# Kernel optimization log

Measured on AMD Instinct MI355X. Metric: run time of the kernel, lower is better.

The kernel has to match this reference:

```python
import jax, jax.numpy as jnp
import numpy as np

G, M, H, HEADS, FFN, MAX_DIST, E = 8, 1024, 256, 8, 1024, 5, 131072
N = G * M
HD = H // HEADS

def _ln(x, g, b, eps=1e-5):
    m = x.mean(-1, keepdims=True)
    v = ((x - m) ** 2).mean(-1, keepdims=True)
    return (x - m) / jnp.sqrt(v + eps) * g + b

def _forward(x, gcn_w, gcn_b, qkv_w, qkv_b, proj_w, proj_b,
             ln1_g, ln1_b, ln2_g, ln2_b, ffn1_w, ffn1_b, ffn2_w, ffn2_b,
             bias_emb, oln1_g, oln1_b, oln2_g, oln2_b,
             offn1_w, offn1_b, offn2_w, offn2_b, edge_index, batch):
    src, dst = edge_index[0], edge_index[1]
    # --- local conv: GCNConv (self-loops + symmetric normalization) ---
    sl = jnp.arange(N, dtype=src.dtype)
    s2 = jnp.concatenate([src, sl]); d2 = jnp.concatenate([dst, sl])
    xw = x @ gcn_w.T
    deg = jax.ops.segment_sum(jnp.ones_like(d2, dtype=x.dtype), d2, num_segments=N)
    dinv = jnp.where(deg > 0, 1.0 / jnp.sqrt(deg), 0.0)
    norm = dinv[s2] * dinv[d2]
    x_local = jax.ops.segment_sum(xw[s2] * norm[:, None], d2, num_segments=N) + gcn_b
    # --- to_dense_batch ---
    counts = jax.ops.segment_sum(jnp.ones(N, jnp.int32), batch, num_segments=G)
    starts = jnp.concatenate([jnp.zeros(1, jnp.int32), jnp.cumsum(counts)[:-1]])
    local = jnp.arange(N, dtype=jnp.int32) - starts[batch]
    dense_x = jnp.zeros((G, M, H), x.dtype).at[batch, local].set(x)
    mask = jnp.zeros((G, M), bool).at[batch, local].set(True)
    # --- SPD via batched boolean adjacency powering (== per-node BFS capped at MAX_DIST) ---
    g_e = batch[src]
    valid = (batch[src] == batch[dst]) & (src != dst)
    ls, ld = local[src], local[dst]
    adj = jnp.zeros((G, M, M), bool).at[g_e, ls, ld].max(valid).at[g_e, ld, ls].max(valid)
    dist = jnp.full((G, M, M), MAX_DIST + 1, jnp.int32)
    eye = jnp.eye(M, dtype=bool)[None]
    dist = jnp.where(eye & mask[:, :, None], 0, dist)
    reach = adj
    dist = jnp.where(reach, jnp.minimum(dist, 1), dist)
    for d in range(2, MAX_DIST + 1):
        reach = jnp.einsum('gij,gjk->gik', reach.astype(x.dtype), adj.astype(x.dtype)) > 0
        dist = jnp.where(reach, jnp.minimum(dist, d), dist)
    attn_bias = bias_emb[dist][..., 0]  # [G, M, M]
    # --- Graphormer encoder layer (layers=1) ---
    h = dense_x
    qkv = (h @ qkv_w.T + qkv_b).reshape(G, M, 3, HEADS, HD).transpose(2, 0, 3, 1, 4)
    q, k, v = qkv[0], qkv[1], qkv[2]  # [G, heads, M, hd]
    scores = jnp.einsum('ghqd,ghkd->ghqk', q, k) * (HD ** -0.5)
    scores = scores + attn_bias[:, None].astype(scores.dtype)
    pad = ~mask
    scores = jnp.where(pad[:, None, None, :], -jnp.inf, scores)
    attn = jax.nn.softmax(scores, axis=-1)
    out = jnp.einsum('ghqk,ghkd->ghqd', attn, v).transpose(0, 2, 1, 3).reshape(G, M, H)
    out = out @ proj_w.T + proj_b
    h = _ln(h + out, ln1_g, ln1_b)
    ff = jax.nn.gelu(h @ ffn1_w.T + ffn1_b, approximate=False) @ ffn2_w.T + ffn2_b
    h = _ln(h + ff, ln2_g, ln2_b)
    h = jnp.where(pad[..., None], 0.0, h)
    x_global = h[batch, local]
    # --- GPS combine + outer FFN (dropout = identity at eval) ---
    y = _ln(x + (x_local + x_global), oln1_g, oln1_b)
    ff2 = jax.nn.gelu(y @ offn1_w.T + offn1_b, approximate=False) @ offn2_w.T + offn2_b
    return _ln(y + ff2, oln2_g, oln2_b)

def setup_inputs() -> dict:
    key = jax.random.key(0)
    ks = jax.random.split(key, 16)
    w = lambda k, *s: jax.random.normal(k, s, jnp.float32) * 0.02
    src = jax.random.randint(ks[0], (E,), 0, N, jnp.int32)
    # keep each edge inside one graph (graphs are contiguous blocks of M nodes)
    dst = (src // M) * M + jax.random.randint(ks[1], (E,), 0, M, jnp.int32)
    return dict(
        x=jax.random.normal(ks[2], (N, H), jnp.float32),
        gcn_w=w(ks[3], H, H), gcn_b=jnp.zeros((H,), jnp.float32),
        qkv_w=w(ks[4], 3 * H, H), qkv_b=jnp.zeros((3 * H,), jnp.float32),
        proj_w=w(ks[5], H, H), proj_b=jnp.zeros((H,), jnp.float32),
        ln1_g=jnp.ones((H,), jnp.float32), ln1_b=jnp.zeros((H,), jnp.float32),
        ln2_g=jnp.ones((H,), jnp.float32), ln2_b=jnp.zeros((H,), jnp.float32),
        ffn1_w=w(ks[6], FFN, H), ffn1_b=jnp.zeros((FFN,), jnp.float32),
        ffn2_w=w(ks[7], H, FFN), ffn2_b=jnp.zeros((H,), jnp.float32),
        bias_emb=w(ks[8], MAX_DIST + 2, 1),
        oln1_g=jnp.ones((H,), jnp.float32), oln1_b=jnp.zeros((H,), jnp.float32),
        oln2_g=jnp.ones((H,), jnp.float32), oln2_b=jnp.zeros((H,), jnp.float32),
        offn1_w=w(ks[9], FFN, H), offn1_b=jnp.zeros((FFN,), jnp.float32),
        offn2_w=w(ks[10], H, FFN), offn2_b=jnp.zeros((H,), jnp.float32),
        edge_index=jnp.stack([src, dst]),
        batch=(jnp.arange(N, dtype=jnp.int32) // M),
    )

def reference(x, gcn_w, gcn_b, qkv_w, qkv_b, proj_w, proj_b,
              ln1_g, ln1_b, ln2_g, ln2_b, ffn1_w, ffn1_b, ffn2_w, ffn2_b,
              bias_emb, oln1_g, oln1_b, oln2_g, oln2_b,
              offn1_w, offn1_b, offn2_w, offn2_b, edge_index, batch):
    return _forward(x, gcn_w, gcn_b, qkv_w, qkv_b, proj_w, proj_b,
                    ln1_g, ln1_b, ln2_g, ln2_b, ffn1_w, ffn1_b, ffn2_w, ffn2_b,
                    bias_emb, oln1_g, oln1_b, oln2_g, oln2_b,
                    offn1_w, offn1_b, offn2_w, offn2_b, edge_index, batch)
```

## Files before the change

kernel.cpp:

```cpp
#include <hip/hip_runtime.h>
#include <hip/hip_bf16.h>
#include <cstdint>

#define G 8
#define M 1024
#define H 256
#define HEADS 8
#define FFND 1024
#define NE 131072
#define NN (G*M)
#define HD 32

typedef unsigned long long u64;
typedef uint8_t u8;
typedef unsigned short ushort_t;
typedef __attribute__((ext_vector_type(8))) short bf16x8;
typedef __attribute__((ext_vector_type(4))) float f32x4;

__device__ __forceinline__ short f2b(float v) {
  __hip_bfloat16 h = __float2bfloat16(v);
  return *reinterpret_cast<short*>(&h);
}
__device__ __forceinline__ float b2f(unsigned int u) {
  union { float f; unsigned int i; } v; v.i = u << 16; return v.f;
}

typedef __attribute__((address_space(1))) const void gvoid;
typedef __attribute__((address_space(3))) void lvoid;
__device__ __forceinline__ void gload16(const void* g, void* l) {
  __builtin_amdgcn_global_load_lds((gvoid*)g, (lvoid*)l, 16, 0, 0);
}

__global__ void k_prep(const int* __restrict__ srcv, const int* __restrict__ dstv,
                       int* __restrict__ deg, int* __restrict__ deg2) {
  int e = blockIdx.x * 256 + threadIdx.x;
  if (e >= NE) return;
  int d = dstv[e], s = srcv[e];
  atomicAdd(&deg[d], 1);
  if (s != d) { atomicAdd(&deg2[s], 1); atomicAdd(&deg2[d], 1); }
}

__global__ __launch_bounds__(1024) void k_scan2(const int* __restrict__ deg, const int* __restrict__ deg2,
                                                int* __restrict__ starts, int* __restrict__ starts2,
                                                float* __restrict__ dinv) {
  __shared__ int tmp[1024];
  const int* in = blockIdx.x ? deg2 : deg;
  int* outp = blockIdx.x ? starts2 : starts;
  int t = threadIdx.x;
  int base = t * 8;
  int v[8]; int s = 0;
  #pragma unroll
  for (int i = 0; i < 8; ++i) { v[i] = in[base + i]; s += v[i]; }
  if (blockIdx.x == 0) {
    #pragma unroll
    for (int i = 0; i < 8; ++i) dinv[base + i] = rsqrtf((float)(v[i] + 1));
  }
  tmp[t] = s;
  __syncthreads();
  for (int off = 1; off < 1024; off <<= 1) {
    int x = (t >= off) ? tmp[t - off] : 0;
    __syncthreads();
    tmp[t] += x;
    __syncthreads();
  }
  int ex = (t == 0) ? 0 : tmp[t - 1];
  #pragma unroll
  for (int i = 0; i < 8; ++i) { outp[base + i] = ex; ex += v[i]; }
}

__global__ void k_fillb(const int* __restrict__ srcv, const int* __restrict__ dstv,
                        const int* __restrict__ starts, int* __restrict__ cursor,
                        int* __restrict__ csr,
                        const int* __restrict__ starts2, int* __restrict__ cur2,
                        int* __restrict__ nbr) {
  int e = blockIdx.x * 256 + threadIdx.x;
  if (e >= NE) return;
  int d = dstv[e], s = srcv[e];
  int pos = atomicAdd(&cursor[d], 1);
  csr[starts[d] + pos] = s;
  if (s != d) {
    int p = atomicAdd(&cur2[s], 1); nbr[starts2[s] + p] = d;
    p = atomicAdd(&cur2[d], 1);     nbr[starts2[d] + p] = s;
  }
}

__global__ __launch_bounds__(256) void k_gather(const int* __restrict__ csr,
    const int* __restrict__ starts, const int* __restrict__ deg,
    const float* __restrict__ dinv, const ushort_t* __restrict__ xwb,
    const float* __restrict__ gcn_b, float* __restrict__ xloc) {
  int d = blockIdx.x, t = threadIdx.x;
  int s0 = starts[d], cnt = deg[d];
  float acc = 0.f;
  for (int j = 0; j < cnt; ++j) {
    int s = csr[s0 + j];
    acc += dinv[s] * b2f(xwb[(size_t)s * H + t]);
  }
  float di = dinv[d];
  float self = b2f(xwb[(size_t)d * H + t]);
  xloc[(size_t)d * H + t] = di * acc + di * di * self + gcn_b[t];
}

__global__ __launch_bounds__(1024) void k_spdm(const int* __restrict__ starts2,
                                               const int* __restrict__ deg2,
                                               const int* __restrict__ nbr,
                                               u8* __restrict__ dist) {
  __shared__ unsigned int Abuf[1024], Bbuf[1024];
  __shared__ u8 dtile[1024][32];
  const int g = blockIdx.x >> 5, w = blockIdx.x & 31;
  const int i = threadIdx.x;
  const int gi = (g << 10) | i;
  unsigned int self = ((i >> 5) == w) ? (1u << (i & 31)) : 0u;
  Abuf[i] = self;
  uint4 six; six.x = six.y = six.z = six.w = 0x06060606u;
  *reinterpret_cast<uint4*>(&dtile[i][0])  = six;
  *reinterpret_cast<uint4*>(&dtile[i][16]) = six;
  if (self) dtile[i][i & 31] = 0;
  const int s0 = starts2[gi], cnt = deg2[gi];
  unsigned int* prev = Abuf;
  unsigned int* cur  = Bbuf;
  unsigned int vis = self;
  __syncthreads();
  for (int l = 1; l <= 5; ++l) {
    unsigned int acc = vis;
    for (int e = 0; e < cnt; ++e)
      acc |= prev[nbr[s0 + e] & 1023];
    unsigned int newly = acc & ~vis;
    while (newly) {
      int k = __ffs(newly) - 1;
      newly &= newly - 1;
      dtile[i][k] = (u8)l;
    }
    cur[i] = acc;
    vis = acc;
    __syncthreads();
    unsigned int* tsw = prev; prev = cur; cur = tsw;
  }
  u8* drow = dist + ((size_t)gi << 10) + w * 32;
  *reinterpret_cast<uint4*>(drow)      = *reinterpret_cast<const uint4*>(&dtile[i][0]);
  *reinterpret_cast<uint4*>(drow + 16) = *reinterpret_cast<const uint4*>(&dtile[i][16]);
}

#define WB_GCN   0
#define WB_QKV   65536
#define WB_PROJ  262144
#define WB_FFN1  327680
#define WB_FFN2  589824
#define WB_OFFN1 851968
#define WB_OFFN2 1114112
#define WB_TOTAL 1376256
#define NXBLK 2048
#define NWBLK 5376

__global__ void k_cvtall(const float* __restrict__ x,
                         const float* p0, const float* p1, const float* p2,
                         const float* p3, const float* p4, const float* p5, const float* p6,
                         const float* __restrict__ qkv_b,
                         ushort_t* __restrict__ x_bf, ushort_t* __restrict__ w_bf,
                         float* __restrict__ bias_cat) {
  int bid = blockIdx.x, t = threadIdx.x;
  if (bid < NXBLK) {
    int i = bid * 256 + t;
    float4 v = reinterpret_cast<const float4*>(x)[i];
    unsigned int lo = (unsigned int)(ushort_t)f2b(v.x) | ((unsigned int)(ushort_t)f2b(v.y) << 16);
    unsigned int hi = (unsigned int)(ushort_t)f2b(v.z) | ((unsigned int)(ushort_t)f2b(v.w) << 16);
    reinterpret_cast<uint2*>(x_bf)[i] = make_uint2(lo, hi);
  } else if (bid < NXBLK + NWBLK) {
    int i = (bid - NXBLK) * 256 + t;
    const float* src; int off;
    if (i < WB_QKV)        { src = p0; off = i; }
    else if (i < WB_PROJ)  { src = p1; off = i - WB_QKV; }
    else if (i < WB_FFN1)  { src = p2; off = i - WB_PROJ; }
    else if (i < WB_FFN2)  { src = p3; off = i - WB_FFN1; }
    else if (i < WB_OFFN1) { src = p4; off = i - WB_FFN2; }
    else if (i < WB_OFFN2) { src = p5; off = i - WB_OFFN1; }
    else                   { src = p6; off = i - WB_OFFN2; }
    w_bf[i] = (ushort_t)f2b(src[off]);
  } else {
    for (int i = t; i < 1024; i += 256) bias_cat[i] = (i < 256) ? 0.f : qkv_b[i - 256];
  }
}

template<int BM, int ACT, int OMODE>
__global__ __launch_bounds__(256) void k_mgemm(const short* __restrict__ A,
                                               const short* __restrict__ W,
                                               const float* __restrict__ bias,
                                               short* __restrict__ Cb,
                                               short* __restrict__ Cb2,
                                               int K, int O) {
  constexpr int FM = BM / 32;
  __shared__ __attribute__((aligned(16))) short As[BM * 64];
  __shared__ __attribute__((aligned(16))) short Ws[64 * 64];
  const int tid = threadIdx.x;
  const int lane = tid & 63, wbase = tid & 192;
  const int wid = tid >> 6;
  const int lg = lane >> 4, lr = lane & 15;
  const int wm = wid >> 1, wn = wid & 1;
  const int m0 = blockIdx.y * BM, n0 = blockIdx.x * 64;
  f32x4 acc[FM][2];
  #pragma unroll
  for (int i = 0; i < FM; ++i)
    #pragma unroll
    for (int j = 0; j < 2; ++j)
      acc[i][j] = (f32x4){0.f, 0.f, 0.f, 0.f};

  for (int k0 = 0; k0 < K; k0 += 64) {
    #pragma unroll
    for (int c = 0; c < BM / 32; ++c) {
      int chunk = c * 256 + tid;
      int row = chunk >> 3, ks = chunk & 7;
      int srcks = ks ^ (row & 7);
      gload16(A + (size_t)(m0 + row) * K + k0 + srcks * 8,
              (char*)As + (c * 256 + wbase) * 16);
    }
    #pragma unroll
    for (int c = 0; c < 2; ++c) {
      int chunk = c * 256 + tid;
      int row = chunk >> 3, ks = chunk & 7;
      int srcks = ks ^ (row & 7);
      gload16(W + (size_t)(n0 + row) * K + k0 + srcks * 8,
              (char*)Ws + (c * 256 + wbase) * 16);
    }
    __syncthreads();
    #pragma unroll
    for (int kk = 0; kk < 2; ++kk) {
      const int d = kk * 4 + lg;
      bf16x8 b[2];
      #pragma unroll
      for (int fn = 0; fn < 2; ++fn) {
        int r = wn * 32 + fn * 16 + lr;
        b[fn] = *reinterpret_cast<const bf16x8*>((const char*)Ws + r * 128 + ((d ^ (r & 7)) * 16));
      }
      #pragma unroll
      for (int fm = 0; fm < FM; ++fm) {
        int r = wm * (BM / 2) + fm * 16 + lr;
        bf16x8 a = *reinterpret_cast<const bf16x8*>((const char*)As + r * 128 + ((d ^ (r & 7)) * 16));
        acc[fm][0] = __builtin_amdgcn_mfma_f32_16x16x32_bf16(a, b[0], acc[fm][0], 0, 0, 0);
        acc[fm][1] = __builtin_amdgcn_mfma_f32_16x16x32_bf16(a, b[1], acc[fm][1], 0, 0, 0);
      }
    }
    __syncthreads();
  }
  #pragma unroll
  for (int fm = 0; fm < FM; ++fm)
    #pragma unroll
    for (int fn = 0; fn < 2; ++fn)
      #pragma unroll
      for (int rg = 0; rg < 4; ++rg) {
        int r = m0 + wm * (BM / 2) + fm * 16 + lg * 4 + rg;
        int cc = n0 + wn * 32 + fn * 16 + lr;
        float v = acc[fm][fn][rg] + (bias ? bias[cc] : 0.f);
        if (ACT == 1) v = 0.5f * v * (1.0f + erff(v * 0.70710678118654752f));
        if (OMODE == 1) Cb[(size_t)r * O + cc] = f2b(v);
        else {
          if (cc < 256) Cb2[(size_t)r * 256 + cc] = f2b(v);
          else          Cb[(size_t)r * 768 + cc - 256] = f2b(v);
        }
      }
}

template<int KK, int OUTB, int LN2>
__global__ __launch_bounds__(512) void k_gemmln(const short* __restrict__ A,
                                                const short* __restrict__ W,
                                                const float* __restrict__ bias,
                                                const float* __restrict__ res1,
                                                const float* __restrict__ gam,
                                                const float* __restrict__ bet,
                                                const float* __restrict__ res2a,
                                                const float* __restrict__ res2b,
                                                const float* __restrict__ gam2,
                                                const float* __restrict__ bet2,
                                                float* __restrict__ outf,
                                                ushort_t* __restrict__ outb) {
  __shared__ __attribute__((aligned(16))) short As[2][32 * 64];
  __shared__ __attribute__((aligned(16))) short Ws[2][256 * 64];
  __shared__ float redS[4][32], redQ[4][32];
  const int tid = threadIdx.x, lane = tid & 63;
  const int hg = tid >> 8, ht = tid & 255;
  const int cw = (tid >> 6) & 3;
  const int lg = lane >> 4, lr = lane & 15;
  const int m0 = blockIdx.x * 32;
  f32x4 acc[2][4];
  #pragma unroll
  for (int i = 0; i < 2; ++i)
    #pragma unroll
    for (int j = 0; j < 4; ++j)
      acc[i][j] = (f32x4){0.f, 0.f, 0.f, 0.f};

  for (int st = 0; st < KK / 128; ++st) {
    const int k0 = hg * (KK / 2) + st * 64;
    {
      int row = ht >> 3, ks = ht & 7, srcks = ks ^ (row & 7);
      gload16(A + (size_t)(m0 + row) * KK + k0 + srcks * 8,
              (char*)As[hg] + (ht & 192) * 16);
    }
    #pragma unroll
    for (int c = 0; c < 8; ++c) {
      int chunk = c * 256 + ht;
      int row = chunk >> 3, ks = chunk & 7;
      int srcks = ks ^ (row & 7);
      gload16(W + (size_t)row * KK + k0 + srcks * 8,
              (char*)Ws[hg] + (c * 256 + (ht & 192)) * 16);
    }
    __syncthreads();
    #pragma unroll
    for (int kk = 0; kk < 2; ++kk) {
      const int d = kk * 4 + lg;
      bf16x8 a[2];
      #pragma unroll
      for (int fr = 0; fr < 2; ++fr) {
        int r = fr * 16 + lr;
        a[fr] = *reinterpret_cast<const bf16x8*>((const char*)As[hg] + r * 128 + ((d ^ (r & 7)) * 16));
      }
      #pragma unroll
      for (int fc = 0; fc < 4; ++fc) {
        int r = cw * 64 + fc * 16 + lr;
        bf16x8 b = *reinterpret_cast<const bf16x8*>((const char*)Ws[hg] + r * 128 + ((d ^ (r & 7)) * 16));
        acc[0][fc] = __builtin_amdgcn_mfma_f32_16x16x32_bf16(a[0], b, acc[0][fc], 0, 0, 0);
        acc[1][fc] = __builtin_amdgcn_mfma_f32_16x16x32_bf16(a[1], b, acc[1][fc], 0, 0, 0);
      }
    }
    __syncthreads();
  }

  float* xch = reinterpret_cast<float*>(&Ws[0][0]);
  if (hg == 1) {
    float* p = xch + ht * 33;
    #pragma unroll
    for (int fr = 0; fr < 2; ++fr)
      #pragma unroll
      for (int fc = 0; fc < 4; ++fc)
        #pragma unroll
        for (int rg = 0; rg < 4; ++rg)
          p[(fr * 4 + fc) * 4 + rg] = acc[fr][fc][rg];
  }
  __syncthreads();

  float vs[2][4][4];
  float mean1[2][4], rstd1[2][4];
  if (hg == 0) {
    float* p = xch + ht * 33;
    float ps[2][4], pq[2][4];
    #pragma unroll
    for (int fr = 0; fr < 2; ++fr)
      #pragma unroll
      for (int rg = 0; rg < 4; ++rg) { ps[fr][rg] = 0.f; pq[fr][rg] = 0.f; }
    #pragma unroll
    for (int fc = 0; fc < 4; ++fc) {
      int col = cw * 64 + fc * 16 + lr;
      float bv = bias[col];
      #pragma unroll
      for (int fr = 0; fr < 2; ++fr)
        #pragma unroll
        for (int rg = 0; rg < 4; ++rg) {
          int row = m0 + fr * 16 + 4 * lg + rg;
          float v = acc[fr][fc][rg] + p[(fr * 4 + fc) * 4 + rg] + bv
                  + res1[(size_t)row * 256 + col];
          vs[fr][fc][rg] = v;
          ps[fr][rg] += v; pq[fr][rg] += v * v;
        }
    }
    #pragma unroll
    for (int fr = 0; fr < 2; ++fr)
      #pragma unroll
      for (int rg = 0; rg < 4; ++rg) {
        float s = ps[fr][rg], q = pq[fr][rg];
        s += __shfl_xor(s, 1); q += __shfl_xor(q, 1);
        s += __shfl_xor(s, 2); q += __shfl_xor(q, 2);
        s += __shfl_xor(s, 4); q += __shfl_xor(q, 4);
        s += __shfl_xor(s, 8); q += __shfl_xor(q, 8);
        if (lr == 0) {
          redS[cw][fr * 16 + 4 * lg + rg] = s;
          redQ[cw][fr * 16 + 4 * lg + rg] = q;
        }
      }
  }
  __syncthreads();
  if (hg == 0) {
    #pragma unroll
    for (int fr = 0; fr < 2; ++fr)
      #pragma unroll
      for (int rg = 0; rg < 4; ++rg) {
        int rl = fr * 16 + 4 * lg + rg;
        float S = redS[0][rl] + redS[1][rl] + redS[2][rl] + redS[3][rl];
        float Q = redQ[0][rl] + redQ[1][rl] + redQ[2][rl] + redQ[3][rl];
        float mn = S * (1.0f / 256.0f);
        mean1[fr][rg] = mn;
        rstd1[fr][rg] = rsqrtf(Q * (1.0f / 256.0f) - mn * mn + 1e-5f);
      }
  }

  if (LN2) {
    __syncthreads();
    if (hg == 0) {
      float ps[2][4], pq[2][4];
      #pragma unroll
      for (int fr = 0; fr < 2; ++fr)
        #pragma unroll
        for (int rg = 0; rg < 4; ++rg) { ps[fr][rg] = 0.f; pq[fr][rg] = 0.f; }
      #pragma unroll
      for (int fc = 0; fc < 4; ++fc) {
        int col = cw * 64 + fc * 16 + lr;
        float g1 = gam[col], b1 = bet[col];
        #pragma unroll
        for (int fr = 0; fr < 2; ++fr)
          #pragma unroll
          for (int rg = 0; rg < 4; ++rg) {
            int row = m0 + fr * 16 + 4 * lg + rg;
            float v1n = (vs[fr][fc][rg] - mean1[fr][rg]) * rstd1[fr][rg] * g1 + b1;
            float v = v1n + res2a[(size_t)row * 256 + col] + res2b[(size_t)row * 256 + col];
            vs[fr][fc][rg] = v;
            ps[fr][rg] += v; pq[fr][rg] += v * v;
          }
      }
      #pragma unroll
      for (int fr = 0; fr < 2; ++fr)
        #pragma unroll
        for (int rg = 0; rg < 4; ++rg) {
          float s = ps[fr][rg], q = pq[fr][rg];
          s += __shfl_xor(s, 1); q += __shfl_xor(q, 1);
          s += __shfl_xor(s, 2); q += __shfl_xor(q, 2);
          s += __shfl_xor(s, 4); q += __shfl_xor(q, 4);
          s += __shfl_xor(s, 8); q += __shfl_xor(q, 8);
          if (lr == 0) {
            redS[cw][fr * 16 + 4 * lg + rg] = s;
            redQ[cw][fr * 16 + 4 * lg + rg] = q;
          }
        }
    }
    __syncthreads();
    if (hg == 0) {
      #pragma unroll
      for (int fr = 0; fr < 2; ++fr)
        #pragma unroll
        for (int rg = 0; rg < 4; ++rg) {
          int rl = fr * 16 + 4 * lg + rg;
          float S = redS[0][rl] + redS[1][rl] + redS[2][rl] + redS[3][rl];
          float Q = redQ[0][rl] + redQ[1][rl] + redQ[2][rl] + redQ[3][rl];
          float mn = S * (1.0f / 256.0f);
          mean1[fr][rg] = mn;
          rstd1[fr][rg] = rsqrtf(Q * (1.0f / 256.0f) - mn * mn + 1e-5f);
        }
    }
  }

  if (hg == 0) {
    const float* gma = LN2 ? gam2 : gam;
    const float* bta = LN2 ? bet2 : bet;
    #pragma unroll
    for (int fr = 0; fr < 2; ++fr)
      #pragma unroll
      for (int rg = 0; rg < 4; ++rg) {
        int rl = fr * 16 + 4 * lg + rg;
        #pragma unroll
        for (int fc = 0; fc < 4; ++fc) {
          int col = cw * 64 + fc * 16 + lr;
          float v = (vs[fr][fc][rg] - mean1[fr][rg]) * rstd1[fr][rg] * gma[col] + bta[col];
          size_t o = (size_t)(m0 + rl) * 256 + col;
          outf[o] = v;
          if (OUTB) outb[o] = (ushort_t)f2b(v);
        }
      }
  }
}

__global__ __launch_bounds__(256) void k_attn(const ushort_t* __restrict__ qkv,
                                              const u8* __restrict__ dist,
                                              const float* __restrict__ emb,
                                              float* __restrict__ po0,
                                              float* __restrict__ po1,
                                              float* __restrict__ pl) {
  __shared__ __attribute__((aligned(16))) char KsB[32 * 128];
  __shared__ __attribute__((aligned(16))) char VtB[32 * 128 + 64];
  __shared__ __attribute__((aligned(16))) char PB[4][16 * 128];
  __shared__ __attribute__((aligned(16))) u8 Ds[32 * 128];
  __shared__ float semb[8];
  const int g = blockIdx.z, head = blockIdx.y;
  const int sp = blockIdx.x >> 4, qblk = blockIdx.x & 15;
  const int q0 = qblk * 64;
  const int kt0 = sp * 8;
  const int t = threadIdx.x, lane = t & 63, wid = t >> 6;
  const int lg = lane >> 4, lr = lane & 15;
  if (t < 7) semb[t] = emb[t] * 1.44269504088896341f;
  const size_t nodebase = (size_t)(g * M) * 768;
  const float C1 = 0.17677669529663687f * 1.44269504088896341f;

  bf16x8 qfrag = *reinterpret_cast<const bf16x8*>(
      qkv + nodebase + (size_t)(q0 + wid * 16 + lr) * 768 + head * 32 + lg * 8);

  const int srow = t >> 2, sc = t & 3;
  const int prow8 = t >> 3, pslot = (t & 7) ^ (prow8 & 7);
  uint4 kr, vr, dr;
  {
    size_t kn = nodebase + (size_t)(kt0 * 64 + srow) * 768 + head * 32;
    kr = *reinterpret_cast<const uint4*>(qkv + kn + 256 + sc * 8);
    vr = *reinterpret_cast<const uint4*>(qkv + kn + 512 + sc * 8);
    dr = *reinterpret_cast<const uint4*>(dist + (size_t)(g * M + kt0 * 64 + srow) * M + q0 + sc * 16);
  }

  f32x4 o0 = {0.f, 0.f, 0.f, 0.f}, o1 = {0.f, 0.f, 0.f, 0.f};
  float lpart[4] = {0.f, 0.f, 0.f, 0.f};
  char* pb = PB[wid];
  const int kp = srow >> 1;
  const int odd = srow & 1;
  const int d0 = sc * 8;
  int r8f[4], slK[4], slD[4];
  #pragma unroll
  for (int fn = 0; fn < 4; ++fn) {
    r8f[fn] = fn * 8 + (lr >> 1);
    slK[fn] = (((lr & 1) << 2) | lg) ^ (r8f[fn] & 7);
    slD[fn] = (((lr & 1) << 2) | wid) ^ (r8f[fn] & 7);
  }

  for (int kt = kt0; kt < kt0 + 8; ++kt) {
    *reinterpret_cast<uint4*>(KsB + prow8 * 128 + pslot * 16) = kr;
    *reinterpret_cast<uint4*>(Ds + prow8 * 128 + pslot * 16) = dr;
    {
      uint4 pvr;
      pvr.x = (unsigned int)__shfl_xor((int)vr.x, 4);
      pvr.y = (unsigned int)__shfl_xor((int)vr.y, 4);
      pvr.z = (unsigned int)__shfl_xor((int)vr.z, 4);
      pvr.w = (unsigned int)__shfl_xor((int)vr.w, 4);
      unsigned int ev[4], ov[4];
      ev[0] = odd ? pvr.x : vr.x; ev[1] = odd ? pvr.y : vr.y;
      ev[2] = odd ? pvr.z : vr.z; ev[3] = odd ? pvr.w : vr.w;
      ov[0] = odd ? vr.x : pvr.x; ov[1] = odd ? vr.y : pvr.y;
      ov[2] = odd ? vr.z : pvr.z; ov[3] = odd ? vr.w : pvr.w;
      #pragma unroll
      for (int di = 0; di < 4; ++di) {
        int dd = odd * 4 + di;
        int d = d0 + dd;
        unsigned int e16 = (dd & 1) ? (ev[dd >> 1] >> 16) : (ev[dd >> 1] & 0xffff);
        unsigned int o16 = (dd & 1) ? (ov[dd >> 1] >> 16) : (ov[dd >> 1] & 0xffff);
        *reinterpret_cast<unsigned int*>(VtB + d * 128 + ((d >> 3) << 4) + ((kp << 2) ^ ((d & 7) << 4)))
            = e16 | (o16 << 16);
      }
    }
    __syncthreads();

    {
      int ktn = (kt + 1) & 15;
      size_t kn = nodebase + (size_t)(ktn * 64 + srow) * 768 + head * 32;
      kr = *reinterpret_cast<const uint4*>(qkv + kn + 256 + sc * 8);
      vr = *reinterpret_cast<const uint4*>(qkv + kn + 512 + sc * 8);
      dr = *reinterpret_cast<const uint4*>(dist + (size_t)(g * M + ktn * 64 + srow) * M + q0 + sc * 16);
    }

    f32x4 s[4];
    unsigned int d4[4];
    #pragma unroll
    for (int fn = 0; fn < 4; ++fn) {
      bf16x8 b = *reinterpret_cast<const bf16x8*>(KsB + r8f[fn] * 128 + slK[fn] * 16);
      s[fn] = __builtin_amdgcn_mfma_f32_16x16x32_bf16(qfrag, b, (f32x4){0.f,0.f,0.f,0.f}, 0, 0, 0);
      d4[fn] = *reinterpret_cast<const unsigned int*>(Ds + r8f[fn] * 128 + slD[fn] * 16 + 4 * lg);
    }
    #pragma unroll
    for (int fn = 0; fn < 4; ++fn)
      #pragma unroll
      for (int rg = 0; rg < 4; ++rg)
        s[fn][rg] = exp2f(s[fn][rg] * C1 + semb[(d4[fn] >> (8 * rg)) & 255]);
    #pragma unroll
    for (int rg = 0; rg < 4; ++rg)
      lpart[rg] += (s[0][rg] + s[1][rg]) + (s[2][rg] + s[3][rg]);

    #pragma unroll
    for (int fn = 0; fn < 4; ++fn)
      #pragma unroll
      for (int rg = 0; rg < 4; ++rg) {
        int qq = 4 * lg + rg, key = fn * 16 + lr;
        *reinterpret_cast<ushort_t*>(pb + qq * 128 + ((key * 2) ^ ((qq & 7) << 4))) =
            (ushort_t)f2b(s[fn][rg]);
      }

    #pragma unroll
    for (int kh = 0; kh < 2; ++kh) {
      int c = kh * 4 + lg;
      int chx = (c << 4) ^ ((lr & 7) << 4);
      bf16x8 a  = *reinterpret_cast<const bf16x8*>(pb + lr * 128 + chx);
      bf16x8 b0 = *reinterpret_cast<const bf16x8*>(VtB + lr * 128 + ((lr >> 3) << 4) + chx);
      bf16x8 b1 = *reinterpret_cast<const bf16x8*>(VtB + (16 + lr) * 128 + (((16 + lr) >> 3) << 4) + chx);
      o0 = __builtin_amdgcn_mfma_f32_16x16x32_bf16(a, b0, o0, 0, 0, 0);
      o1 = __builtin_amdgcn_mfma_f32_16x16x32_bf16(a, b1, o1, 0, 0, 0);
    }
    __syncthreads();
  }

  float* po = sp ? po1 : po0;
  #pragma unroll
  for (int rg = 0; rg < 4; ++rg) {
    float l = lpart[rg];
    l += __shfl_xor(l, 1);
    l += __shfl_xor(l, 2);
    l += __shfl_xor(l, 4);
    l += __shfl_xor(l, 8);
    int q = q0 + wid * 16 + 4 * lg + rg;
    size_t qn = (size_t)(g * M + q);
    po[qn * H + head * 32 + lr]      = o0[rg];
    po[qn * H + head * 32 + 16 + lr] = o1[rg];
    if (lr == 0)
      pl[(sp << 16) + ((g * HEADS + head) << 10) + q] = l;
  }
}

__global__ __launch_bounds__(256) void k_acomb(const float* __restrict__ po0,
                                               const float* __restrict__ po1,
                                               const float* __restrict__ pl,
                                               ushort_t* __restrict__ attno) {
  int i4 = blockIdx.x * 256 + threadIdx.x;
  int idx = i4 * 4;
  int q = idx >> 8;
  int col = idx & 255;
  int head = col >> 5;
  int g = q >> 10, ql = q & 1023;
  int li = ((g * HEADS + head) << 10) + ql;
  float inv = 1.0f / (pl[li] + pl[65536 + li]);
  float4 a = reinterpret_cast<const float4*>(po0)[i4];
  float4 b = reinterpret_cast<const float4*>(po1)[i4];
  unsigned int lo = (unsigned int)(ushort_t)f2b((a.x + b.x) * inv)
                  | ((unsigned int)(ushort_t)f2b((a.y + b.y) * inv) << 16);
  unsigned int hi = (unsigned int)(ushort_t)f2b((a.z + b.z) * inv)
                  | ((unsigned int)(ushort_t)f2b((a.w + b.w) * inv) << 16);
  reinterpret_cast<uint2*>(attno)[i4] = make_uint2(lo, hi);
}

extern "C" void kernel_launch(void* const* d_in, const int* in_sizes, int n_in,
                              void* d_out, int out_size, void* d_ws, size_t ws_size,
                              hipStream_t stream) {
  const float* x      = (const float*)d_in[0];
  const float* gcn_w  = (const float*)d_in[1];
  const float* gcn_b  = (const float*)d_in[2];
  const float* qkv_w  = (const float*)d_in[3];
  const float* qkv_b  = (const float*)d_in[4];
  const float* proj_w = (const float*)d_in[5];
  const float* proj_b = (const float*)d_in[6];
  const float* ln1_g  = (const float*)d_in[7];
  const float* ln1_b  = (const float*)d_in[8];
  const float* ln2_g  = (const float*)d_in[9];
  const float* ln2_b  = (const float*)d_in[10];
  const float* ffn1_w = (const float*)d_in[11];
  const float* ffn1_b = (const float*)d_in[12];
  const float* ffn2_w = (const float*)d_in[13];
  const float* ffn2_b = (const float*)d_in[14];
  const float* bias_e = (const float*)d_in[15];
  const float* oln1_g = (const float*)d_in[16];
  const float* oln1_b = (const float*)d_in[17];
  const float* oln2_g = (const float*)d_in[18];
  const float* oln2_b = (const float*)d_in[19];
  const float* offn1_w= (const float*)d_in[20];
  const float* offn1_b= (const float*)d_in[21];
  const float* offn2_w= (const float*)d_in[22];
  const float* offn2_b= (const float*)d_in[23];
  const int*   eidx   = (const int*)d_in[24];
  const int* esrc = eidx;
  const int* edst = eidx + NE;

  char* wsp = (char*)d_ws;
  size_t off = 0;
  auto alloc = [&](size_t bytes) { void* p = wsp + off; off += (bytes + 255) & ~255ull; return p; };
  const size_t SZ_NH = (size_t)NN * H * 4;
  ushort_t* x_bf  = (ushort_t*)alloc((size_t)NN * H * 2);
  ushort_t* w_bf  = (ushort_t*)alloc((size_t)WB_TOTAL * 2);
  float* bias_cat = (float*)alloc(1024 * 4);
  ushort_t* xwb   = (ushort_t*)alloc((size_t)NN * H * 2);
  float* xloc = (float*)alloc(SZ_NH);
  float* dinv = (float*)alloc((size_t)NN * 4);
  int*   deg  = (int*)  alloc((size_t)NN * 4);
  int* cursor = (int*)  alloc((size_t)NN * 4);
  int*  deg2  = (int*)  alloc((size_t)NN * 4);
  int* cursor2= (int*)  alloc((size_t)NN * 4);
  int* starts = (int*)  alloc((size_t)NN * 4);
  int* starts2= (int*)  alloc((size_t)NN * 4);
  int*   csr  = (int*)  alloc((size_t)NE * 4);
  int*   nbr  = (int*)  alloc((size_t)2 * NE * 4);
  u8*    dist = (u8*)   alloc((size_t)NN * M);
  ushort_t* qkvb = (ushort_t*)alloc((size_t)NN * 768 * 2);
  float* h1   = (float*)alloc(SZ_NH);
  ushort_t* h1_bf = (ushort_t*)alloc((size_t)NN * H * 2);
  float* y    = (float*)alloc(SZ_NH);
  float* pl   = (float*)alloc((size_t)2 * 65536 * 4);

  ushort_t* attno = x_bf;
  ushort_t* mid = (ushort_t*)dist;
  ushort_t* y_bf = h1_bf;
  float* po0 = h1;
  float* po1 = y;
  float* outp = (float*)d_out;

  ushort_t* proj_wb = w_bf + WB_PROJ;
  ushort_t* ffn1_wb = w_bf + WB_FFN1;
  ushort_t* ffn2_wb = w_bf + WB_FFN2;
  ushort_t* offn1_wb= w_bf + WB_OFFN1;
  ushort_t* offn2_wb= w_bf + WB_OFFN2;

  hipMemsetAsync(deg, 0, (size_t)4 * NN * 4, stream);

  k_cvtall<<<NXBLK + NWBLK + 1, 256, 0, stream>>>(x, gcn_w, qkv_w, proj_w, ffn1_w,
                                                  ffn2_w, offn1_w, offn2_w, qkv_b,
                                                  x_bf, w_bf, bias_cat);

  k_prep<<<NE / 256, 256, 0, stream>>>(esrc, edst, deg, deg2);
  k_scan2<<<2, 1024, 0, stream>>>(deg, deg2, starts, starts2, dinv);
  k_fillb<<<NE / 256, 256, 0, stream>>>(esrc, edst, starts, cursor, csr, starts2, cursor2, nbr);

  k_mgemm<128, 0, 2><<<dim3(1024 / 64, NN / 128), 256, 0, stream>>>(
      (const short*)x_bf, (const short*)w_bf, bias_cat, (short*)qkvb, (short*)xwb, 256, 1024);
  k_gather<<<NN, 256, 0, stream>>>(csr, starts, deg, dinv, xwb, gcn_b, xloc);

  k_spdm<<<G * 32, 1024, 0, stream>>>(starts2, deg2, nbr, dist);

  k_attn<<<dim3(32, HEADS, G), 256, 0, stream>>>(qkvb, dist, bias_e, po0, po1, pl);
  k_acomb<<<NN * H / 4 / 256, 256, 0, stream>>>(po0, po1, pl, attno);

  k_gemmln<256, 1, 0><<<NN / 32, 512, 0, stream>>>(
      (const short*)attno, (const short*)proj_wb, proj_b, x, ln1_g, ln1_b,
      nullptr, nullptr, nullptr, nullptr, h1, h1_bf);
  k_mgemm<128, 1, 1><<<dim3(FFND / 64, NN / 128), 256, 0, stream>>>(
      (const short*)h1_bf, (const short*)ffn1_wb, ffn1_b, (short*)mid, nullptr, 256, FFND);
  k_gemmln<1024, 1, 1><<<NN / 32, 512, 0, stream>>>(
      (const short*)mid, (const short*)ffn2_wb, ffn2_b, h1, ln2_g, ln2_b,
      x, xloc, oln1_g, oln1_b, y, y_bf);
  k_mgemm<128, 1, 1><<<dim3(FFND / 64, NN / 128), 256, 0, stream>>>(
      (const short*)y_bf, (const short*)offn1_wb, offn1_b, (short*)mid, nullptr, 256, FFND);
  k_gemmln<1024, 0, 0><<<NN / 32, 512, 0, stream>>>(
      (const short*)mid, (const short*)offn2_wb, offn2_b, y, oln2_g, oln2_b,
      nullptr, nullptr, nullptr, nullptr, outp, nullptr);
}
```

Measured before the change: 361.2 us.

## Emit transposed V from QKV GEMM and fold degree counting into convert kernel

```diff
diff --git a/kernel.cpp b/kernel.cpp
--- a/kernel.cpp
+++ b/kernel.cpp
@@ -29,15 +29,6 @@
 typedef __attribute__((address_space(3))) void lvoid;
 __device__ __forceinline__ void gload16(const void* g, void* l) {
   __builtin_amdgcn_global_load_lds((gvoid*)g, (lvoid*)l, 16, 0, 0);
-}
-
-__global__ void k_prep(const int* __restrict__ srcv, const int* __restrict__ dstv,
-                       int* __restrict__ deg, int* __restrict__ deg2) {
-  int e = blockIdx.x * 256 + threadIdx.x;
-  if (e >= NE) return;
-  int d = dstv[e], s = srcv[e];
-  atomicAdd(&deg[d], 1);
-  if (s != d) { atomicAdd(&deg2[s], 1); atomicAdd(&deg2[d], 1); }
 }
 
 __global__ __launch_bounds__(1024) void k_scan2(const int* __restrict__ deg, const int* __restrict__ deg2,
@@ -91,6 +82,7 @@
   int d = blockIdx.x, t = threadIdx.x;
   int s0 = starts[d], cnt = deg[d];
   float acc = 0.f;
+  #pragma unroll 4
   for (int j = 0; j < cnt; ++j) {
     int s = csr[s0 + j];
     acc += dinv[s] * b2f(xwb[(size_t)s * H + t]);
@@ -122,6 +114,7 @@
   __syncthreads();
   for (int l = 1; l <= 5; ++l) {
     unsigned int acc = vis;
+    #pragma unroll 4
     for (int e = 0; e < cnt; ++e)
       acc |= prev[nbr[s0 + e] & 1023];
     unsigned int newly = acc & ~vis;
@@ -150,13 +143,16 @@
 #define WB_TOTAL 1376256
 #define NXBLK 2048
 #define NWBLK 5376
+#define NEBLK 512
 
 __global__ void k_cvtall(const float* __restrict__ x,
                          const float* p0, const float* p1, const float* p2,
                          const float* p3, const float* p4, const float* p5, const float* p6,
                          const float* __restrict__ qkv_b,
                          ushort_t* __restrict__ x_bf, ushort_t* __restrict__ w_bf,
-                         float* __restrict__ bias_cat) {
+                         float* __restrict__ bias_cat,
+                         const int* __restrict__ srcv, const int* __restrict__ dstv,
+                         int* __restrict__ deg, int* __restrict__ deg2) {
   int bid = blockIdx.x, t = threadIdx.x;
   if (bid < NXBLK) {
     int i = bid * 256 + t;
@@ -175,8 +171,13 @@
     else if (i < WB_OFFN2) { src = p5; off = i - WB_OFFN1; }
     else                   { src = p6; off = i - WB_OFFN2; }
     w_bf[i] = (ushort_t)f2b(src[off]);
+  } else if (bid == NXBLK + NWBLK) {
+    for (int i = t; i < 1024; i += 256) bias_cat[i] = (i < 256) ? 0.f : qkv_b[i - 256];
   } else {
-    for (int i = t; i < 1024; i += 256) bias_cat[i] = (i < 256) ? 0.f : qkv_b[i - 256];
+    int e = (bid - NXBLK - NWBLK - 1) * 256 + t;
+    int d = dstv[e], s = srcv[e];
+    atomicAdd(&deg[d], 1);
+    if (s != d) { atomicAdd(&deg2[s], 1); atomicAdd(&deg2[d], 1); }
   }
 }
 
@@ -186,6 +187,7 @@
                                                const float* __restrict__ bias,
                                                short* __restrict__ Cb,
                                                short* __restrict__ Cb2,
+                                               ushort_t* __restrict__ vTp,
                                                int K, int O) {
   constexpr int FM = BM / 32;
   __shared__ __attribute__((aligned(16))) short As[BM * 64];
@@ -243,19 +245,40 @@
   #pragma unroll
   for (int fm = 0; fm < FM; ++fm)
     #pragma unroll
-    for (int fn = 0; fn < 2; ++fn)
+    for (int fn = 0; fn < 2; ++fn) {
+      int cc = n0 + wn * 32 + fn * 16 + lr;
+      float bv = bias ? bias[cc] : 0.f;
+      float tv[4];
       #pragma unroll
       for (int rg = 0; rg < 4; ++rg) {
-        int r = m0 + wm * (BM / 2) + fm * 16 + lg * 4 + rg;
-        int cc = n0 + wn * 32 + fn * 16 + lr;
-        float v = acc[fm][fn][rg] + (bias ? bias[cc] : 0.f);
+        float v = acc[fm][fn][rg] + bv;
         if (ACT == 1) v = 0.5f * v * (1.0f + erff(v * 0.70710678118654752f));
-        if (OMODE == 1) Cb[(size_t)r * O + cc] = f2b(v);
-        else {
-          if (cc < 256) Cb2[(size_t)r * 256 + cc] = f2b(v);
-          else          Cb[(size_t)r * 768 + cc - 256] = f2b(v);
+        tv[rg] = v;
+      }
+      int r0 = m0 + wm * (BM / 2) + fm * 16 + lg * 4;
+      if (OMODE == 1) {
+        #pragma unroll
+        for (int rg = 0; rg < 4; ++rg)
+          Cb[(size_t)(r0 + rg) * O + cc] = f2b(tv[rg]);
+      } else {
+        if (cc < 256) {
+          #pragma unroll
+          for (int rg = 0; rg < 4; ++rg)
+            Cb2[(size_t)(r0 + rg) * 256 + cc] = f2b(tv[rg]);
+        } else if (cc < 768) {
+          #pragma unroll
+          for (int rg = 0; rg < 4; ++rg)
+            Cb[(size_t)(r0 + rg) * 768 + cc - 256] = f2b(tv[rg]);
+        } else {
+          u64 pk = 0;
+          #pragma unroll
+          for (int rg = 0; rg < 4; ++rg)
+            pk |= (u64)(ushort_t)f2b(tv[rg]) << (16 * rg);
+          int gg = r0 >> 10, ql = r0 & 1023;
+          *reinterpret_cast<u64*>(vTp + (((size_t)(gg * 256 + cc - 768)) << 10) + ql) = pk;
         }
       }
+    }
 }
 
 template<int KK, int OUTB, int LN2>
@@ -464,13 +487,14 @@
 }
 
 __global__ __launch_bounds__(256) void k_attn(const ushort_t* __restrict__ qkv,
+                                              const ushort_t* __restrict__ vT,
                                               const u8* __restrict__ dist,
                                               const float* __restrict__ emb,
                                               float* __restrict__ po0,
                                               float* __restrict__ po1,
                                               float* __restrict__ pl) {
   __shared__ __attribute__((aligned(16))) char KsB[32 * 128];
-  __shared__ __attribute__((aligned(16))) char VtB[32 * 128 + 64];
+  __shared__ __attribute__((aligned(16))) char VtB[32 * 128];
   __shared__ __attribute__((aligned(16))) char PB[4][16 * 128];
   __shared__ __attribute__((aligned(16))) u8 Ds[32 * 128];
   __shared__ float semb[8];
@@ -482,27 +506,27 @@
   const int lg = lane >> 4, lr = lane & 15;
   if (t < 7) semb[t] = emb[t] * 1.44269504088896341f;
   const size_t nodebase = (size_t)(g * M) * 768;
+  const size_t vtbase = ((size_t)(g * 256 + head * 32)) << 10;
   const float C1 = 0.17677669529663687f * 1.44269504088896341f;
 
   bf16x8 qfrag = *reinterpret_cast<const bf16x8*>(
       qkv + nodebase + (size_t)(q0 + wid * 16 + lr) * 768 + head * 32 + lg * 8);
 
   const int srow = t >> 2, sc = t & 3;
+  const int vrow = t >> 3, vc = t & 7;
   const int prow8 = t >> 3, pslot = (t & 7) ^ (prow8 & 7);
+  const int vslot = vc ^ (vrow & 7);
   uint4 kr, vr, dr;
   {
     size_t kn = nodebase + (size_t)(kt0 * 64 + srow) * 768 + head * 32;
     kr = *reinterpret_cast<const uint4*>(qkv + kn + 256 + sc * 8);
-    vr = *reinterpret_cast<const uint4*>(qkv + kn + 512 + sc * 8);
+    vr = *reinterpret_cast<const uint4*>(vT + vtbase + ((size_t)vrow << 10) + kt0 * 64 + vc * 8);
     dr = *reinterpret_cast<const uint4*>(dist + (size_t)(g * M + kt0 * 64 + srow) * M + q0 + sc * 16);
   }
 
   f32x4 o0 = {0.f, 0.f, 0.f, 0.f}, o1 = {0.f, 0.f, 0.f, 0.f};
   float lpart[4] = {0.f, 0.f, 0.f, 0.f};
   char* pb = PB[wid];
-  const int kp = srow >> 1;
-  const int odd = srow & 1;
-  const int d0 = sc * 8;
   int r8f[4], slK[4], slD[4];
   #pragma unroll
   for (int fn = 0; fn < 4; ++fn) {
@@ -514,34 +538,14 @@
   for (int kt = kt0; kt < kt0 + 8; ++kt) {
     *reinterpret_cast<uint4*>(KsB + prow8 * 128 + pslot * 16) = kr;
     *reinterpret_cast<uint4*>(Ds + prow8 * 128 + pslot * 16) = dr;
-    {
-      uint4 pvr;
-      pvr.x = (unsigned int)__shfl_xor((int)vr.x, 4);
-      pvr.y = (unsigned int)__shfl_xor((int)vr.y, 4);
-      pvr.z = (unsigned int)__shfl_xor((int)vr.z, 4);
-      pvr.w = (unsigned int)__shfl_xor((int)vr.w, 4);
-      unsigned int ev[4], ov[4];
-      ev[0] = odd ? pvr.x : vr.x; ev[1] = odd ? pvr.y : vr.y;
-      ev[2] = odd ? pvr.z : vr.z; ev[3] = odd ? pvr.w : vr.w;
-      ov[0] = odd ? vr.x : pvr.x; ov[1] = odd ? vr.y : pvr.y;
-      ov[2] = odd ? vr.z : pvr.z; ov[3] = odd ? vr.w : pvr.w;
-      #pragma unroll
-      for (int di = 0; di < 4; ++di) {
-        int dd = odd * 4 + di;
-        int d = d0 + dd;
-        unsigned int e16 = (dd & 1) ? (ev[dd >> 1] >> 16) : (ev[dd >> 1] & 0xffff);
-        unsigned int o16 = (dd & 1) ? (ov[dd >> 1] >> 16) : (ov[dd >> 1] & 0xffff);
-        *reinterpret_cast<unsigned int*>(VtB + d * 128 + ((d >> 3) << 4) + ((kp << 2) ^ ((d & 7) << 4)))
-            = e16 | (o16 << 16);
-      }
-    }
+    *reinterpret_cast<uint4*>(VtB + vrow * 128 + vslot * 16) = vr;
     __syncthreads();
 
     {
       int ktn = (kt + 1) & 15;
       size_t kn = nodebase + (size_t)(ktn * 64 + srow) * 768 + head * 32;
       kr = *reinterpret_cast<const uint4*>(qkv + kn + 256 + sc * 8);
-      vr = *reinterpret_cast<const uint4*>(qkv + kn + 512 + sc * 8);
+      vr = *reinterpret_cast<const uint4*>(vT + vtbase + ((size_t)vrow << 10) + ktn * 64 + vc * 8);
       dr = *reinterpret_cast<const uint4*>(dist + (size_t)(g * M + ktn * 64 + srow) * M + q0 + sc * 16);
     }
 
@@ -574,10 +578,10 @@
     #pragma unroll
     for (int kh = 0; kh < 2; ++kh) {
       int c = kh * 4 + lg;
-      int chx = (c << 4) ^ ((lr & 7) << 4);
+      int chx = ((c ^ (lr & 7)) << 4);
       bf16x8 a  = *reinterpret_cast<const bf16x8*>(pb + lr * 128 + chx);
-      bf16x8 b0 = *reinterpret_cast<const bf16x8*>(VtB + lr * 128 + ((lr >> 3) << 4) + chx);
-      bf16x8 b1 = *reinterpret_cast<const bf16x8*>(VtB + (16 + lr) * 128 + (((16 + lr) >> 3) << 4) + chx);
+      bf16x8 b0 = *reinterpret_cast<const bf16x8*>(VtB + lr * 128 + chx);
+      bf16x8 b1 = *reinterpret_cast<const bf16x8*>(VtB + (16 + lr) * 128 + chx);
       o0 = __builtin_amdgcn_mfma_f32_16x16x32_bf16(a, b0, o0, 0, 0, 0);
       o1 = __builtin_amdgcn_mfma_f32_16x16x32_bf16(a, b1, o1, 0, 0, 0);
     }
@@ -661,6 +665,7 @@
   ushort_t* w_bf  = (ushort_t*)alloc((size_t)WB_TOTAL * 2);
   float* bias_cat = (float*)alloc(1024 * 4);
   ushort_t* xwb   = (ushort_t*)alloc((size_t)NN * H * 2);
+  ushort_t* vT    = (ushort_t*)alloc((size_t)NN * 256 * 2);
   float* xloc = (float*)alloc(SZ_NH);
   float* dinv = (float*)alloc((size_t)NN * 4);
   int*   deg  = (int*)  alloc((size_t)NN * 4);
@@ -693,33 +698,32 @@
 
   hipMemsetAsync(deg, 0, (size_t)4 * NN * 4, stream);
 
-  k_cvtall<<<NXBLK + NWBLK + 1, 256, 0, stream>>>(x, gcn_w, qkv_w, proj_w, ffn1_w,
-                                                  ffn2_w, offn1_w, offn2_w, qkv_b,
-                                                  x_bf, w_bf, bias_cat);
-
-  k_prep<<<NE / 256, 256, 0, stream>>>(esrc, edst, deg, deg2);
+  k_cvtall<<<NXBLK + NWBLK + 1 + NEBLK, 256, 0, stream>>>(
+      x, gcn_w, qkv_w, proj_w, ffn1_w, ffn2_w, offn1_w, offn2_w, qkv_b,
+      x_bf, w_bf, bias_cat, esrc, edst, deg, deg2);
+
   k_scan2<<<2, 1024, 0, stream>>>(deg, deg2, starts, starts2, dinv);
   k_fillb<<<NE / 256, 256, 0, stream>>>(esrc, edst, starts, cursor, csr, starts2, cursor2, nbr);
 
   k_mgemm<128, 0, 2><<<dim3(1024 / 64, NN / 128), 256, 0, stream>>>(
-      (const short*)x_bf, (const short*)w_bf, bias_cat, (short*)qkvb, (short*)xwb, 256, 1024);
+      (const short*)x_bf, (const short*)w_bf, bias_cat, (short*)qkvb, (short*)xwb, vT, 256, 1024);
   k_gather<<<NN, 256, 0, stream>>>(csr, starts, deg, dinv, xwb, gcn_b, xloc);
 
   k_spdm<<<G * 32, 1024, 0, stream>>>(starts2, deg2, nbr, dist);
 
-  k_attn<<<dim3(32, HEADS, G), 256, 0, stream>>>(qkvb, dist, bias_e, po0, po1, pl);
+  k_attn<<<dim3(32, HEADS, G), 256, 0, stream>>>(qkvb, vT, dist, bias_e, po0, po1, pl);
   k_acomb<<<NN * H / 4 / 256, 256, 0, stream>>>(po0, po1, pl, attno);
 
   k_gemmln<256, 1, 0><<<NN / 32, 512, 0, stream>>>(
       (const short*)attno, (const short*)proj_wb, proj_b, x, ln1_g, ln1_b,
       nullptr, nullptr, nullptr, nullptr, h1, h1_bf);
   k_mgemm<128, 1, 1><<<dim3(FFND / 64, NN / 128), 256, 0, stream>>>(
-      (const short*)h1_bf, (const short*)ffn1_wb, ffn1_b, (short*)mid, nullptr, 256, FFND);
+      (const short*)h1_bf, (const short*)ffn1_wb, ffn1_b, (short*)mid, nullptr, nullptr, 256, FFND);
   k_gemmln<1024, 1, 1><<<NN / 32, 512, 0, stream>>>(
       (const short*)mid, (const short*)ffn2_wb, ffn2_b, h1, ln2_g, ln2_b,
       x, xloc, oln1_g, oln1_b, y, y_bf);
   k_mgemm<128, 1, 1><<<dim3(FFND / 64, NN / 128), 256, 0, stream>>>(
-      (const short*)y_bf, (const short*)offn1_wb, offn1_b, (short*)mid, nullptr, 256, FFND);
+      (const short*)y_bf, (const short*)offn1_wb, offn1_b, (short*)mid, nullptr, nullptr, 256, FFND);
   k_gemmln<1024, 0, 0><<<NN / 32, 512, 0, stream>>>(
       (const short*)mid, (const short*)offn2_wb, offn2_b, y, oln2_g, oln2_b,
       nullptr, nullptr, nullptr, nullptr, outp, nullptr);
```

After: 337.5 us. 6.6% less time.
